# Kernel tuning notes

Measured on AMD Instinct MI355X. Metric: run time of the kernel, lower is better.

## Reference

```python
import jax, jax.numpy as jnp
import numpy as np

N_EMBD = 1024
D_K = 1024
D_V = 1024

def setup_inputs() -> dict:
    key = jax.random.key(0)
    k1, k2, k3, k4 = jax.random.split(key, 4)
    B, T = 4, 2048
    std = N_EMBD ** -0.5
    x = jax.random.normal(k1, (B, T, N_EMBD), dtype=jnp.float32)
    Wq = jax.random.normal(k2, (N_EMBD, D_K), dtype=jnp.float32) * std
    Wk = jax.random.normal(k3, (N_EMBD, D_K), dtype=jnp.float32) * std
    Wv = jax.random.normal(k4, (N_EMBD, D_V), dtype=jnp.float32) * std
    return {"x": x, "Wq": Wq, "Wk": Wk, "Wv": Wv}

def reference(x, Wq, Wk, Wv):
    # x: [B, T, C]
    T = x.shape[1]
    q = x @ Wq  # [B, T, d_k]
    k = x @ Wk  # [B, T, d_k]
    v = x @ Wv  # [B, T, d_v]
    scale = Wk.shape[1] ** -0.5
    wei = jnp.einsum('btd,bsd->bts', q, k) * scale  # [B, T, T]
    causal = jnp.tril(jnp.ones((T, T), dtype=bool))
    wei = jnp.where(causal, wei, -jnp.inf)
    wei = jax.nn.softmax(wei, axis=-1)
    return wei @ v  # [B, T, d_v]
```

## Files before the change

### kernel.cpp

```cpp
#include <hip/hip_runtime.h>
#include <hip/hip_bf16.h>
#include <stdint.h>

using bf16_t = __hip_bfloat16;
typedef __bf16 bf16x8 __attribute__((ext_vector_type(8)));
typedef float f32x4 __attribute__((ext_vector_type(4)));

__device__ __forceinline__ void async_lds16(const void* g, void* l) {
  __builtin_amdgcn_global_load_lds(
      (const __attribute__((address_space(1))) void*)g,
      (__attribute__((address_space(3))) void*)l, 16, 0, 0);
}

__device__ __forceinline__ unsigned short f2bf_u16(float f) {
  __hip_bfloat16 h = __float2bfloat16(f);
  return __builtin_bit_cast(unsigned short, h);
}

__global__ __launch_bounds__(256) void convert_x_kernel(
    const float* __restrict__ x, bf16_t* __restrict__ xb) {
  size_t i = ((size_t)blockIdx.x * 256 + threadIdx.x) * 4;
  float4 v = *(const float4*)(x + i);
  ushort4 o;
  o.x = f2bf_u16(v.x);
  o.y = f2bf_u16(v.y);
  o.z = f2bf_u16(v.z);
  o.w = f2bf_u16(v.w);
  *(ushort4*)(xb + i) = o;
}

__global__ __launch_bounds__(256) void convert_transpose_w_kernel(
    const float* __restrict__ Wq, const float* __restrict__ Wk,
    const float* __restrict__ Wv, bf16_t* __restrict__ wt) {
  __shared__ bf16_t tile[32][33];
  const float* W = (blockIdx.z == 0) ? Wq : (blockIdx.z == 1) ? Wk : Wv;
  bf16_t* WT = wt + (size_t)blockIdx.z * 1024 * 1024;
  const int tx = threadIdx.x & 31;
  const int ty = threadIdx.x >> 5;
  const int bx = blockIdx.x & 31;
  const int by = blockIdx.x >> 5;
  const int k0 = by * 32, n0 = bx * 32;
#pragma unroll
  for (int j = 0; j < 32; j += 8)
    tile[ty + j][tx] = __float2bfloat16(W[(size_t)(k0 + ty + j) * 1024 + n0 + tx]);
  __syncthreads();
#pragma unroll
  for (int j = 0; j < 32; j += 8)
    WT[(size_t)(n0 + ty + j) * 1024 + k0 + tx] = tile[tx][ty + j];
}

template <int OUT_MODE, bool CAUSAL_SKIP, bool KLIMIT, bool XCDSWZ>
__global__ __launch_bounds__(512, 2) void gemm_pipe_kernel(
    const bf16_t* __restrict__ A, const bf16_t* __restrict__ BT,
    void* __restrict__ Cv, void* __restrict__ Cv2, void* __restrict__ Cv3,
    int M, int N, int K, int lda, int ldb, int ldc,
    long long aBatch, long long bBatch, long long cBatch) {
  int bx = blockIdx.x, by = blockIdx.y;
  if (XCDSWZ) {
    const int gx = gridDim.x;
    const int nwg = gx * gridDim.y;
    const int id = by * gx + bx;
    const int cpx = nwg >> 3;
    const int swz = (id & 7) * cpx + (id >> 3);
    by = swz / gx;
    bx = swz % gx;
  }
  const int m0 = by * 128;
  const int n0 = bx * 256;
  if (CAUSAL_SKIP && 2 * bx > by) return;
  A += (size_t)blockIdx.z * aBatch;
  BT += (size_t)blockIdx.z * bBatch;
  int nkt = K >> 5;
  if (KLIMIT) {
    int lim = (m0 + 128) >> 5;
    nkt = nkt < lim ? nkt : lim;
  }

  __shared__ bf16_t lsA[3 * 128 * 32];
  __shared__ bf16_t lsB[3 * 256 * 32];

  const int tid = threadIdx.x;
  const int wid = tid >> 6;
  const int lane = tid & 63;
  const int wm = wid >> 2;
  const int wn = wid & 3;

  const int sr = tid >> 2;
  const int ss = tid & 3;
  const int sswz = ss ^ ((sr >> 1) & 3);
  const bf16_t* gA = A + (size_t)(m0 + sr) * lda + sswz * 8;
  const bf16_t* gB0 = BT + (size_t)(n0 + sr) * ldb + sswz * 8;
  const bf16_t* gB1 = BT + (size_t)(n0 + 128 + sr) * ldb + sswz * 8;

  const int kslot = (lane >> 4) ^ ((lane >> 1) & 3);
  const int abase = (wm * 64 + (lane & 15)) * 32 + kslot * 8;
  const int bbase = (wn * 64 + (lane & 15)) * 32 + kslot * 8;

  f32x4 acc[4][4];
  const f32x4 zero = {0.f, 0.f, 0.f, 0.f};
#pragma unroll
  for (int m = 0; m < 4; ++m)
#pragma unroll
    for (int n = 0; n < 4; ++n) acc[m][n] = zero;

  async_lds16(gA, lsA + wid * 512);
  async_lds16(gB0, lsB + wid * 512);
  async_lds16(gB1, lsB + 4096 + wid * 512);
  if (nkt > 1) {
    async_lds16(gA + 32, lsA + 4096 + wid * 512);
    async_lds16(gB0 + 32, lsB + 8192 + wid * 512);
    async_lds16(gB1 + 32, lsB + 8192 + 4096 + wid * 512);
    asm volatile("s_waitcnt vmcnt(3)" ::: "memory");
  } else {
    asm volatile("s_waitcnt vmcnt(0)" ::: "memory");
  }
  __builtin_amdgcn_s_barrier();

  int cb = 0;
  for (int t = 0; t < nkt; ++t) {
    const bf16_t* bufA = lsA + cb * 4096;
    const bf16_t* bufB = lsB + cb * 8192;
    int sb = cb + 2;
    if (sb >= 3) sb -= 3;

    bf16x8 af[4], bfr[4];
#pragma unroll
    for (int mf = 0; mf < 4; ++mf)
      af[mf] = *(const bf16x8*)(bufA + abase + mf * 512);
    bfr[0] = *(const bf16x8*)(bufB + bbase);
    bfr[1] = *(const bf16x8*)(bufB + bbase + 512);
    if (t + 2 < nkt) {
      async_lds16(gA + (t + 2) * 32, lsA + sb * 4096 + wid * 512);
      async_lds16(gB0 + (t + 2) * 32, lsB + sb * 8192 + wid * 512);
    }
    __builtin_amdgcn_s_barrier();
    __builtin_amdgcn_s_setprio(1);
#pragma unroll
    for (int mf = 0; mf < 4; ++mf)
#pragma unroll
      for (int nf = 0; nf < 2; ++nf)
        acc[mf][nf] = __builtin_amdgcn_mfma_f32_16x16x32_bf16(
            af[mf], bfr[nf], acc[mf][nf], 0, 0, 0);
    __builtin_amdgcn_s_setprio(0);
    __builtin_amdgcn_s_barrier();

    bfr[2] = *(const bf16x8*)(bufB + bbase + 1024);
    bfr[3] = *(const bf16x8*)(bufB + bbase + 1536);
    if (t + 2 < nkt)
      async_lds16(gB1 + (t + 2) * 32, lsB + sb * 8192 + 4096 + wid * 512);
    if (t + 2 < nkt) {
      asm volatile("s_waitcnt vmcnt(3)" ::: "memory");
    } else if (t + 2 == nkt) {
      asm volatile("s_waitcnt vmcnt(0)" ::: "memory");
    }
    __builtin_amdgcn_s_barrier();
    __builtin_amdgcn_s_setprio(1);
#pragma unroll
    for (int mf = 0; mf < 4; ++mf)
#pragma unroll
      for (int nf = 2; nf < 4; ++nf)
        acc[mf][nf] = __builtin_amdgcn_mfma_f32_16x16x32_bf16(
            af[mf], bfr[nf], acc[mf][nf], 0, 0, 0);
    __builtin_amdgcn_s_setprio(0);
    __builtin_amdgcn_s_barrier();

    cb = cb + 1;
    if (cb >= 3) cb -= 3;
  }

  const int erow = wm * 64 + (lane >> 4) * 4;
  const int ecol = wn * 64 + (lane & 15);
  if (OUT_MODE == 2) {
    float* C = (float*)Cv + (size_t)blockIdx.z * cBatch;
#pragma unroll
    for (int m = 0; m < 4; ++m)
#pragma unroll
      for (int n = 0; n < 4; ++n)
#pragma unroll
        for (int j = 0; j < 4; ++j) {
          int r = m0 + erow + m * 16 + j;
          int c = n0 + ecol + n * 16;
          C[(size_t)r * ldc + c] = acc[m][n][j];
        }
  } else {
    if (n0 < 2048) {
      bf16_t* C = (bf16_t*)((n0 < 1024) ? Cv : Cv2);
      const int cb0 = n0 & 1023;
#pragma unroll
      for (int m = 0; m < 4; ++m)
#pragma unroll
        for (int n = 0; n < 4; ++n)
#pragma unroll
          for (int j = 0; j < 4; ++j) {
            int r = m0 + erow + m * 16 + j;
            int c = cb0 + ecol + n * 16;
            C[(size_t)r * 1024 + c] = __float2bfloat16(acc[m][n][j]);
          }
    } else {
      bf16_t* C = (bf16_t*)Cv3;
      const int d0 = n0 - 2048;
#pragma unroll
      for (int m = 0; m < 4; ++m)
#pragma unroll
        for (int n = 0; n < 4; ++n)
#pragma unroll
          for (int j = 0; j < 4; ++j) {
            int r = m0 + erow + m * 16 + j;
            int d = d0 + ecol + n * 16;
            int b = r >> 11, tt = r & 2047;
            C[((size_t)b * 1024 + d) * 2048 + tt] = __float2bfloat16(acc[m][n][j]);
          }
    }
  }
}

__global__ __launch_bounds__(256) void softmax_causal_kernel(float* __restrict__ S) {
  const int lane = threadIdx.x & 63;
  const int rg = blockIdx.x * 4 + (threadIdx.x >> 6);
  const int b = rg >> 11;
  const int t = rg & 2047;
  float* srow = S + (size_t)b * 2048 * 2048 + (size_t)t * 2048;

  float4 v[8];
#pragma unroll
  for (int it = 0; it < 8; ++it) v[it] = *(const float4*)(srow + (it * 64 + lane) * 4);

  float mx = -3.0e38f;
#pragma unroll
  for (int it = 0; it < 8; ++it) {
    int s0 = (it * 64 + lane) * 4;
    if (s0 + 0 <= t) mx = fmaxf(mx, v[it].x);
    if (s0 + 1 <= t) mx = fmaxf(mx, v[it].y);
    if (s0 + 2 <= t) mx = fmaxf(mx, v[it].z);
    if (s0 + 3 <= t) mx = fmaxf(mx, v[it].w);
  }
#pragma unroll
  for (int off = 32; off > 0; off >>= 1) mx = fmaxf(mx, __shfl_xor(mx, off, 64));

  const float kMul = 0.03125f * 1.4426950408889634f;
  float p[8][4];
  float sum = 0.f;
#pragma unroll
  for (int it = 0; it < 8; ++it) {
    int s0 = (it * 64 + lane) * 4;
    float e0 = (s0 + 0 <= t) ? exp2f((v[it].x - mx) * kMul) : 0.f;
    float e1 = (s0 + 1 <= t) ? exp2f((v[it].y - mx) * kMul) : 0.f;
    float e2 = (s0 + 2 <= t) ? exp2f((v[it].z - mx) * kMul) : 0.f;
    float e3 = (s0 + 3 <= t) ? exp2f((v[it].w - mx) * kMul) : 0.f;
    p[it][0] = e0; p[it][1] = e1; p[it][2] = e2; p[it][3] = e3;
    sum += (e0 + e1) + (e2 + e3);
  }
#pragma unroll
  for (int off = 32; off > 0; off >>= 1) sum += __shfl_xor(sum, off, 64);
  const float inv = 1.f / sum;

  bf16_t* prow = (bf16_t*)srow;
#pragma unroll
  for (int it = 0; it < 8; ++it) {
    ushort4 o;
    o.x = f2bf_u16(p[it][0] * inv);
    o.y = f2bf_u16(p[it][1] * inv);
    o.z = f2bf_u16(p[it][2] * inv);
    o.w = f2bf_u16(p[it][3] * inv);
    *(ushort4*)(prow + (it * 64 + lane) * 4) = o;
  }
}

extern "C" void kernel_launch(void* const* d_in, const int* in_sizes, int n_in,
                              void* d_out, int out_size, void* d_ws, size_t ws_size,
                              hipStream_t stream) {
  (void)in_sizes; (void)n_in; (void)out_size;
  const float* x = (const float*)d_in[0];
  const float* Wq = (const float*)d_in[1];
  const float* Wk = (const float*)d_in[2];
  const float* Wv = (const float*)d_in[3];
  float* out = (float*)d_out;

  char* ws = (char*)d_ws;
  const size_t NEED = 123731968;
  const bool batched = ws_size >= NEED;

  bf16_t* xb = (bf16_t*)ws;
  float* S;
  bf16_t *WT, *Qb, *Kb, *VT;
  if (batched) {
    S = (float*)ws;
    WT = (bf16_t*)(ws + 67108864);
    Qb = (bf16_t*)(ws + 73400320);
    Kb = (bf16_t*)(ws + 90177536);
    VT = (bf16_t*)(ws + 106954752);
  } else {
    S = (float*)ws;
    WT = (bf16_t*)(ws + 16777216);
    Qb = (bf16_t*)(ws + 16777216 + 6291456);
    Kb = Qb + 8388608;
    VT = Kb + 8388608;
  }

  convert_x_kernel<<<8192, 256, 0, stream>>>(x, xb);
  convert_transpose_w_kernel<<<dim3(1024, 1, 3), 256, 0, stream>>>(Wq, Wk, Wv, WT);

  gemm_pipe_kernel<3, false, false, true><<<dim3(12, 64, 1), 512, 0, stream>>>(
      xb, WT, Qb, Kb, VT, 8192, 3072, 1024, 1024, 1024, 0, 0, 0, 0);

  if (batched) {
    gemm_pipe_kernel<2, true, false, false><<<dim3(8, 16, 4), 512, 0, stream>>>(
        Qb, Kb, S, nullptr, nullptr, 2048, 2048, 1024, 1024, 1024, 2048,
        2097152LL, 2097152LL, 4194304LL);
    softmax_causal_kernel<<<2048, 256, 0, stream>>>(S);
    gemm_pipe_kernel<2, false, true, false><<<dim3(4, 16, 4), 512, 0, stream>>>(
        (const bf16_t*)S, VT, out, nullptr, nullptr, 2048, 1024, 2048, 4096,
        2048, 1024, 8388608LL, 2097152LL, 2097152LL);
  } else {
    for (int b = 0; b < 4; ++b) {
      const size_t qoff = (size_t)b * 2048 * 1024;
      gemm_pipe_kernel<2, true, false, false><<<dim3(8, 16, 1), 512, 0, stream>>>(
          Qb + qoff, Kb + qoff, S, nullptr, nullptr, 2048, 2048, 1024, 1024,
          1024, 2048, 0, 0, 0);
      softmax_causal_kernel<<<512, 256, 0, stream>>>(S);
      gemm_pipe_kernel<2, false, true, false><<<dim3(4, 16, 1), 512, 0, stream>>>(
          (const bf16_t*)S, VT + qoff, out + qoff, nullptr, nullptr, 2048,
          1024, 2048, 4096, 2048, 1024, 0, 0, 0);
    }
  }
}
```

Measured before the change: 187.0 us.

## Enlarge GEMM tiles to 256x256x64 with double-buffered four-phase pipeline

Measured after the change: 200.5 us. 1.07x slower.

```diff
diff --git a/kernel.cpp b/kernel.cpp
--- a/kernel.cpp
+++ b/kernel.cpp
@@ -50,7 +50,7 @@
 }
 
 template <int OUT_MODE, bool CAUSAL_SKIP, bool KLIMIT, bool XCDSWZ>
-__global__ __launch_bounds__(512, 2) void gemm_pipe_kernel(
+__global__ __launch_bounds__(512, 2) void gemm256_kernel(
     const bf16_t* __restrict__ A, const bf16_t* __restrict__ BT,
     void* __restrict__ Cv, void* __restrict__ Cv2, void* __restrict__ Cv3,
     int M, int N, int K, int lda, int ldb, int ldc,
@@ -65,19 +65,19 @@
     by = swz / gx;
     bx = swz % gx;
   }
-  const int m0 = by * 128;
+  const int m0 = by * 256;
   const int n0 = bx * 256;
-  if (CAUSAL_SKIP && 2 * bx > by) return;
+  if (CAUSAL_SKIP && bx > by) return;
   A += (size_t)blockIdx.z * aBatch;
   BT += (size_t)blockIdx.z * bBatch;
-  int nkt = K >> 5;
+  int nkt = K >> 6;
   if (KLIMIT) {
-    int lim = (m0 + 128) >> 5;
+    int lim = (m0 + 256) >> 6;
     nkt = nkt < lim ? nkt : lim;
   }
 
-  __shared__ bf16_t lsA[3 * 128 * 32];
-  __shared__ bf16_t lsB[3 * 256 * 32];
+  __shared__ bf16_t lsA[2 * 16384];
+  __shared__ bf16_t lsB[2 * 16384];
 
   const int tid = threadIdx.x;
   const int wid = tid >> 6;
@@ -86,94 +86,123 @@
   const int wn = wid & 3;
 
   const int sr = tid >> 2;
-  const int ss = tid & 3;
-  const int sswz = ss ^ ((sr >> 1) & 3);
-  const bf16_t* gA = A + (size_t)(m0 + sr) * lda + sswz * 8;
+  const int sswz = (tid & 3) ^ ((tid >> 3) & 3);
+  const bf16_t* gA0 = A + (size_t)(m0 + sr) * lda + sswz * 8;
+  const bf16_t* gA1 = A + (size_t)(m0 + 128 + sr) * lda + sswz * 8;
   const bf16_t* gB0 = BT + (size_t)(n0 + sr) * ldb + sswz * 8;
   const bf16_t* gB1 = BT + (size_t)(n0 + 128 + sr) * ldb + sswz * 8;
 
-  const int kslot = (lane >> 4) ^ ((lane >> 1) & 3);
-  const int abase = (wm * 64 + (lane & 15)) * 32 + kslot * 8;
-  const int bbase = (wn * 64 + (lane & 15)) * 32 + kslot * 8;
-
-  f32x4 acc[4][4];
+  auto stageA = [&](int t, int kh) {
+    bf16_t* d = lsA + ((t & 1) << 14) + (kh << 13) + (wid << 9);
+    const size_t co = (size_t)(t << 6) + (kh << 5);
+    async_lds16(gA0 + co, d);
+    async_lds16(gA1 + co, d + 4096);
+  };
+  auto stageB = [&](int t, int kh) {
+    bf16_t* d = lsB + ((t & 1) << 14) + (kh << 13) + (wid << 9);
+    const size_t co = (size_t)(t << 6) + (kh << 5);
+    async_lds16(gB0 + co, d);
+    async_lds16(gB1 + co, d + 4096);
+  };
+
+  const int kswz = ((lane >> 4) ^ ((lane >> 1) & 3)) * 8;
+  const int aRd = (wm * 128 + (lane & 15)) * 32 + kswz;
+  const int bRd = (wn * 64 + (lane & 15)) * 32 + kswz;
+
+  f32x4 acc[8][4];
   const f32x4 zero = {0.f, 0.f, 0.f, 0.f};
 #pragma unroll
-  for (int m = 0; m < 4; ++m)
+  for (int m = 0; m < 8; ++m)
 #pragma unroll
     for (int n = 0; n < 4; ++n) acc[m][n] = zero;
 
-  async_lds16(gA, lsA + wid * 512);
-  async_lds16(gB0, lsB + wid * 512);
-  async_lds16(gB1, lsB + 4096 + wid * 512);
+  stageA(0, 0);
+  stageB(0, 0);
+  stageA(0, 1);
+  stageB(0, 1);
   if (nkt > 1) {
-    async_lds16(gA + 32, lsA + 4096 + wid * 512);
-    async_lds16(gB0 + 32, lsB + 8192 + wid * 512);
-    async_lds16(gB1 + 32, lsB + 8192 + 4096 + wid * 512);
-    asm volatile("s_waitcnt vmcnt(3)" ::: "memory");
+    stageA(1, 0);
+    stageB(1, 0);
+    asm volatile("s_waitcnt vmcnt(4)" ::: "memory");
   } else {
     asm volatile("s_waitcnt vmcnt(0)" ::: "memory");
   }
   __builtin_amdgcn_s_barrier();
 
-  int cb = 0;
+  bf16x8 af[4], bfr[4];
+
+#define PHASE_TAIL()                                      \
+  __builtin_amdgcn_s_barrier();                           \
+  asm volatile("s_waitcnt lgkmcnt(0)" ::: "memory");      \
+  __builtin_amdgcn_sched_barrier(0);                      \
+  __builtin_amdgcn_s_setprio(1);
+
+#define MFMA16(mh)                                        \
+  _Pragma("unroll") for (int mf = 0; mf < 4; ++mf)        \
+      _Pragma("unroll") for (int nf = 0; nf < 4; ++nf)    \
+          acc[(mh)*4 + mf][nf] = __builtin_amdgcn_mfma_f32_16x16x32_bf16( \
+              af[mf], bfr[nf], acc[(mh)*4 + mf][nf], 0, 0, 0);
+
   for (int t = 0; t < nkt; ++t) {
-    const bf16_t* bufA = lsA + cb * 4096;
-    const bf16_t* bufB = lsB + cb * 8192;
-    int sb = cb + 2;
-    if (sb >= 3) sb -= 3;
-
-    bf16x8 af[4], bfr[4];
+    const bf16_t* bufA = lsA + ((t & 1) << 14);
+    const bf16_t* bufB = lsB + ((t & 1) << 14);
+
+#pragma unroll
+    for (int nf = 0; nf < 4; ++nf)
+      bfr[nf] = *(const bf16x8*)(bufB + (nf << 9) + bRd);
 #pragma unroll
     for (int mf = 0; mf < 4; ++mf)
-      af[mf] = *(const bf16x8*)(bufA + abase + mf * 512);
-    bfr[0] = *(const bf16x8*)(bufB + bbase);
-    bfr[1] = *(const bf16x8*)(bufB + bbase + 512);
-    if (t + 2 < nkt) {
-      async_lds16(gA + (t + 2) * 32, lsA + sb * 4096 + wid * 512);
-      async_lds16(gB0 + (t + 2) * 32, lsB + sb * 8192 + wid * 512);
-    }
-    __builtin_amdgcn_s_barrier();
-    __builtin_amdgcn_s_setprio(1);
-#pragma unroll
-    for (int mf = 0; mf < 4; ++mf)
-#pragma unroll
-      for (int nf = 0; nf < 2; ++nf)
-        acc[mf][nf] = __builtin_amdgcn_mfma_f32_16x16x32_bf16(
-            af[mf], bfr[nf], acc[mf][nf], 0, 0, 0);
+      af[mf] = *(const bf16x8*)(bufA + (mf << 9) + aRd);
+    if (t + 1 < nkt) stageA(t + 1, 1);
+    PHASE_TAIL()
+    MFMA16(0)
     __builtin_amdgcn_s_setprio(0);
     __builtin_amdgcn_s_barrier();
 
-    bfr[2] = *(const bf16x8*)(bufB + bbase + 1024);
-    bfr[3] = *(const bf16x8*)(bufB + bbase + 1536);
-    if (t + 2 < nkt)
-      async_lds16(gB1 + (t + 2) * 32, lsB + sb * 8192 + 4096 + wid * 512);
+#pragma unroll
+    for (int mf = 0; mf < 4; ++mf)
+      af[mf] = *(const bf16x8*)(bufA + ((mf + 4) << 9) + aRd);
+    if (t + 1 < nkt) stageB(t + 1, 1);
+    PHASE_TAIL()
+    MFMA16(1)
+    __builtin_amdgcn_s_setprio(0);
+    __builtin_amdgcn_s_barrier();
+
+#pragma unroll
+    for (int nf = 0; nf < 4; ++nf)
+      bfr[nf] = *(const bf16x8*)(bufB + 8192 + (nf << 9) + bRd);
+#pragma unroll
+    for (int mf = 0; mf < 4; ++mf)
+      af[mf] = *(const bf16x8*)(bufA + 8192 + (mf << 9) + aRd);
+    if (t + 2 < nkt) stageA(t + 2, 0);
+    PHASE_TAIL()
+    MFMA16(0)
+    __builtin_amdgcn_s_setprio(0);
+    __builtin_amdgcn_s_barrier();
+
+#pragma unroll
+    for (int mf = 0; mf < 4; ++mf)
+      af[mf] = *(const bf16x8*)(bufA + 8192 + ((mf + 4) << 9) + aRd);
+    if (t + 2 < nkt) stageB(t + 2, 0);
+    PHASE_TAIL()
+    MFMA16(1)
+    __builtin_amdgcn_s_setprio(0);
     if (t + 2 < nkt) {
-      asm volatile("s_waitcnt vmcnt(3)" ::: "memory");
-    } else if (t + 2 == nkt) {
+      asm volatile("s_waitcnt vmcnt(4)" ::: "memory");
+    } else if (t + 1 < nkt) {
       asm volatile("s_waitcnt vmcnt(0)" ::: "memory");
     }
     __builtin_amdgcn_s_barrier();
-    __builtin_amdgcn_s_setprio(1);
-#pragma unroll
-    for (int mf = 0; mf < 4; ++mf)
-#pragma unroll
-      for (int nf = 2; nf < 4; ++nf)
-        acc[mf][nf] = __builtin_amdgcn_mfma_f32_16x16x32_bf16(
-            af[mf], bfr[nf], acc[mf][nf], 0, 0, 0);
-    __builtin_amdgcn_s_setprio(0);
-    __builtin_amdgcn_s_barrier();
-
-    cb = cb + 1;
-    if (cb >= 3) cb -= 3;
-  }
-
-  const int erow = wm * 64 + (lane >> 4) * 4;
+  }
+#undef PHASE_TAIL
+#undef MFMA16
+
+  const int erow = wm * 128 + (lane >> 4) * 4;
   const int ecol = wn * 64 + (lane & 15);
   if (OUT_MODE == 2) {
     float* C = (float*)Cv + (size_t)blockIdx.z * cBatch;
 #pragma unroll
-    for (int m = 0; m < 4; ++m)
+    for (int m = 0; m < 8; ++m)
 #pragma unroll
       for (int n = 0; n < 4; ++n)
 #pragma unroll
@@ -187,7 +216,7 @@
       bf16_t* C = (bf16_t*)((n0 < 1024) ? Cv : Cv2);
       const int cb0 = n0 & 1023;
 #pragma unroll
-      for (int m = 0; m < 4; ++m)
+      for (int m = 0; m < 8; ++m)
 #pragma unroll
         for (int n = 0; n < 4; ++n)
 #pragma unroll
@@ -200,7 +229,7 @@
       bf16_t* C = (bf16_t*)Cv3;
       const int d0 = n0 - 2048;
 #pragma unroll
-      for (int m = 0; m < 4; ++m)
+      for (int m = 0; m < 8; ++m)
 #pragma unroll
         for (int n = 0; n < 4; ++n)
 #pragma unroll
@@ -220,10 +249,16 @@
   const int b = rg >> 11;
   const int t = rg & 2047;
   float* srow = S + (size_t)b * 2048 * 2048 + (size_t)t * 2048;
+  const int qmax = t >> 8;
 
   float4 v[8];
 #pragma unroll
-  for (int it = 0; it < 8; ++it) v[it] = *(const float4*)(srow + (it * 64 + lane) * 4);
+  for (int it = 0; it < 8; ++it) {
+    if (it <= qmax)
+      v[it] = *(const float4*)(srow + (it * 64 + lane) * 4);
+    else
+      v[it] = make_float4(0.f, 0.f, 0.f, 0.f);
+  }
 
   float mx = -3.0e38f;
 #pragma unroll
@@ -257,12 +292,14 @@
   bf16_t* prow = (bf16_t*)srow;
 #pragma unroll
   for (int it = 0; it < 8; ++it) {
-    ushort4 o;
-    o.x = f2bf_u16(p[it][0] * inv);
-    o.y = f2bf_u16(p[it][1] * inv);
-    o.z = f2bf_u16(p[it][2] * inv);
-    o.w = f2bf_u16(p[it][3] * inv);
-    *(ushort4*)(prow + (it * 64 + lane) * 4) = o;
+    if (it <= qmax) {
+      ushort4 o;
+      o.x = f2bf_u16(p[it][0] * inv);
+      o.y = f2bf_u16(p[it][1] * inv);
+      o.z = f2bf_u16(p[it][2] * inv);
+      o.w = f2bf_u16(p[it][3] * inv);
+      *(ushort4*)(prow + (it * 64 + lane) * 4) = o;
+    }
   }
 }
 
@@ -300,25 +337,25 @@
   convert_x_kernel<<<8192, 256, 0, stream>>>(x, xb);
   convert_transpose_w_kernel<<<dim3(1024, 1, 3), 256, 0, stream>>>(Wq, Wk, Wv, WT);
 
-  gemm_pipe_kernel<3, false, false, true><<<dim3(12, 64, 1), 512, 0, stream>>>(
+  gemm256_kernel<3, false, false, true><<<dim3(12, 32, 1), 512, 0, stream>>>(
       xb, WT, Qb, Kb, VT, 8192, 3072, 1024, 1024, 1024, 0, 0, 0, 0);
 
   if (batched) {
-    gemm_pipe_kernel<2, true, false, false><<<dim3(8, 16, 4), 512, 0, stream>>>(
+    gemm256_kernel<2, true, false, false><<<dim3(8, 8, 4), 512, 0, stream>>>(
         Qb, Kb, S, nullptr, nullptr, 2048, 2048, 1024, 1024, 1024, 2048,
         2097152LL, 2097152LL, 4194304LL);
     softmax_causal_kernel<<<2048, 256, 0, stream>>>(S);
-    gemm_pipe_kernel<2, false, true, false><<<dim3(4, 16, 4), 512, 0, stream>>>(
+    gemm256_kernel<2, false, true, false><<<dim3(4, 8, 4), 512, 0, stream>>>(
         (const bf16_t*)S, VT, out, nullptr, nullptr, 2048, 1024, 2048, 4096,
         2048, 1024, 8388608LL, 2097152LL, 2097152LL);
   } else {
     for (int b = 0; b < 4; ++b) {
       const size_t qoff = (size_t)b * 2048 * 1024;
-      gemm_pipe_kernel<2, true, false, false><<<dim3(8, 16, 1), 512, 0, stream>>>(
+      gemm256_kernel<2, true, false, false><<<dim3(8, 8, 1), 512, 0, stream>>>(
           Qb + qoff, Kb + qoff, S, nullptr, nullptr, 2048, 2048, 1024, 1024,
           1024, 2048, 0, 0, 0);
       softmax_causal_kernel<<<512, 256, 0, stream>>>(S);
-      gemm_pipe_kernel<2, false, true, false><<<dim3(4, 16, 1), 512, 0, stream>>>(
+      gemm256_kernel<2, false, true, false><<<dim3(4, 8, 1), 512, 0, stream>>>(
           (const bf16_t*)S, VT + qoff, out + qoff, nullptr, nullptr, 2048,
           1024, 2048, 4096, 2048, 1024, 0, 0, 0);
     }
```

## Store attention scores as bf16, skip masked softmax tiles, merge conversion kernels

Applied to the files above, without the earlier changes.

New measurement: 179.9 us. 3.8% less time.

```diff
diff --git a/kernel.cpp b/kernel.cpp
--- a/kernel.cpp
+++ b/kernel.cpp
@@ -17,28 +17,37 @@
   return __builtin_bit_cast(unsigned short, h);
 }
 
-__global__ __launch_bounds__(256) void convert_x_kernel(
-    const float* __restrict__ x, bf16_t* __restrict__ xb) {
-  size_t i = ((size_t)blockIdx.x * 256 + threadIdx.x) * 4;
-  float4 v = *(const float4*)(x + i);
-  ushort4 o;
-  o.x = f2bf_u16(v.x);
-  o.y = f2bf_u16(v.y);
-  o.z = f2bf_u16(v.z);
-  o.w = f2bf_u16(v.w);
-  *(ushort4*)(xb + i) = o;
-}
-
-__global__ __launch_bounds__(256) void convert_transpose_w_kernel(
+__device__ __forceinline__ float bf2f(unsigned short u) {
+  __hip_bfloat16 h = __builtin_bit_cast(__hip_bfloat16, u);
+  return __bfloat162float(h);
+}
+
+__global__ __launch_bounds__(256) void convert_all_kernel(
+    const float* __restrict__ x, bf16_t* __restrict__ xb,
     const float* __restrict__ Wq, const float* __restrict__ Wk,
     const float* __restrict__ Wv, bf16_t* __restrict__ wt) {
   __shared__ bf16_t tile[32][33];
-  const float* W = (blockIdx.z == 0) ? Wq : (blockIdx.z == 1) ? Wk : Wv;
-  bf16_t* WT = wt + (size_t)blockIdx.z * 1024 * 1024;
+  const int bid = blockIdx.x;
+  if (bid < 8192) {
+    size_t i = ((size_t)bid * 256 + threadIdx.x) * 4;
+    float4 v = *(const float4*)(x + i);
+    ushort4 o;
+    o.x = f2bf_u16(v.x);
+    o.y = f2bf_u16(v.y);
+    o.z = f2bf_u16(v.z);
+    o.w = f2bf_u16(v.w);
+    *(ushort4*)(xb + i) = o;
+    return;
+  }
+  const int w = bid - 8192;
+  const int z = w >> 10;
+  const int bxy = w & 1023;
+  const float* W = (z == 0) ? Wq : (z == 1) ? Wk : Wv;
+  bf16_t* WT = wt + (size_t)z * 1024 * 1024;
   const int tx = threadIdx.x & 31;
   const int ty = threadIdx.x >> 5;
-  const int bx = blockIdx.x & 31;
-  const int by = blockIdx.x >> 5;
+  const int bx = bxy & 31;
+  const int by = bxy >> 5;
   const int k0 = by * 32, n0 = bx * 32;
 #pragma unroll
   for (int j = 0; j < 32; j += 8)
@@ -182,6 +191,18 @@
           int c = n0 + ecol + n * 16;
           C[(size_t)r * ldc + c] = acc[m][n][j];
         }
+  } else if (OUT_MODE == 4) {
+    bf16_t* C = (bf16_t*)Cv + (size_t)blockIdx.z * cBatch;
+#pragma unroll
+    for (int m = 0; m < 4; ++m)
+#pragma unroll
+      for (int n = 0; n < 4; ++n)
+#pragma unroll
+        for (int j = 0; j < 4; ++j) {
+          int r = m0 + erow + m * 16 + j;
+          int c = n0 + ecol + n * 16;
+          C[(size_t)r * ldc + c] = __float2bfloat16(acc[m][n][j]);
+        }
   } else {
     if (n0 < 2048) {
       bf16_t* C = (bf16_t*)((n0 < 1024) ? Cv : Cv2);
@@ -214,25 +235,36 @@
   }
 }
 
-__global__ __launch_bounds__(256) void softmax_causal_kernel(float* __restrict__ S) {
+__global__ __launch_bounds__(256) void softmax_causal_kernel(bf16_t* __restrict__ Sb) {
   const int lane = threadIdx.x & 63;
   const int rg = blockIdx.x * 4 + (threadIdx.x >> 6);
   const int b = rg >> 11;
   const int t = rg & 2047;
-  float* srow = S + (size_t)b * 2048 * 2048 + (size_t)t * 2048;
-
-  float4 v[8];
-#pragma unroll
-  for (int it = 0; it < 8; ++it) v[it] = *(const float4*)(srow + (it * 64 + lane) * 4);
+  bf16_t* srow = Sb + (size_t)b * 8388608 + (size_t)t * 4096;
+  const int qmax = t >> 8;
+
+  float v[8][4];
+#pragma unroll
+  for (int it = 0; it < 8; ++it) {
+    if (it <= qmax) {
+      ushort4 u = *(const ushort4*)(srow + (it * 64 + lane) * 4);
+      v[it][0] = bf2f(u.x);
+      v[it][1] = bf2f(u.y);
+      v[it][2] = bf2f(u.z);
+      v[it][3] = bf2f(u.w);
+    } else {
+      v[it][0] = v[it][1] = v[it][2] = v[it][3] = 0.f;
+    }
+  }
 
   float mx = -3.0e38f;
 #pragma unroll
   for (int it = 0; it < 8; ++it) {
     int s0 = (it * 64 + lane) * 4;
-    if (s0 + 0 <= t) mx = fmaxf(mx, v[it].x);
-    if (s0 + 1 <= t) mx = fmaxf(mx, v[it].y);
-    if (s0 + 2 <= t) mx = fmaxf(mx, v[it].z);
-    if (s0 + 3 <= t) mx = fmaxf(mx, v[it].w);
+    if (s0 + 0 <= t) mx = fmaxf(mx, v[it][0]);
+    if (s0 + 1 <= t) mx = fmaxf(mx, v[it][1]);
+    if (s0 + 2 <= t) mx = fmaxf(mx, v[it][2]);
+    if (s0 + 3 <= t) mx = fmaxf(mx, v[it][3]);
   }
 #pragma unroll
   for (int off = 32; off > 0; off >>= 1) mx = fmaxf(mx, __shfl_xor(mx, off, 64));
@@ -243,10 +275,10 @@
 #pragma unroll
   for (int it = 0; it < 8; ++it) {
     int s0 = (it * 64 + lane) * 4;
-    float e0 = (s0 + 0 <= t) ? exp2f((v[it].x - mx) * kMul) : 0.f;
-    float e1 = (s0 + 1 <= t) ? exp2f((v[it].y - mx) * kMul) : 0.f;
-    float e2 = (s0 + 2 <= t) ? exp2f((v[it].z - mx) * kMul) : 0.f;
-    float e3 = (s0 + 3 <= t) ? exp2f((v[it].w - mx) * kMul) : 0.f;
+    float e0 = (s0 + 0 <= t) ? exp2f((v[it][0] - mx) * kMul) : 0.f;
+    float e1 = (s0 + 1 <= t) ? exp2f((v[it][1] - mx) * kMul) : 0.f;
+    float e2 = (s0 + 2 <= t) ? exp2f((v[it][2] - mx) * kMul) : 0.f;
+    float e3 = (s0 + 3 <= t) ? exp2f((v[it][3] - mx) * kMul) : 0.f;
     p[it][0] = e0; p[it][1] = e1; p[it][2] = e2; p[it][3] = e3;
     sum += (e0 + e1) + (e2 + e3);
   }
@@ -254,15 +286,16 @@
   for (int off = 32; off > 0; off >>= 1) sum += __shfl_xor(sum, off, 64);
   const float inv = 1.f / sum;
 
-  bf16_t* prow = (bf16_t*)srow;
 #pragma unroll
   for (int it = 0; it < 8; ++it) {
-    ushort4 o;
-    o.x = f2bf_u16(p[it][0] * inv);
-    o.y = f2bf_u16(p[it][1] * inv);
-    o.z = f2bf_u16(p[it][2] * inv);
-    o.w = f2bf_u16(p[it][3] * inv);
-    *(ushort4*)(prow + (it * 64 + lane) * 4) = o;
+    if (it <= qmax) {
+      ushort4 o;
+      o.x = f2bf_u16(p[it][0] * inv);
+      o.y = f2bf_u16(p[it][1] * inv);
+      o.z = f2bf_u16(p[it][2] * inv);
+      o.w = f2bf_u16(p[it][3] * inv);
+      *(ushort4*)(srow + (it * 64 + lane) * 4) = o;
+    }
   }
 }
 
@@ -281,45 +314,44 @@
   const bool batched = ws_size >= NEED;
 
   bf16_t* xb = (bf16_t*)ws;
-  float* S;
+  bf16_t* Sb;
   bf16_t *WT, *Qb, *Kb, *VT;
   if (batched) {
-    S = (float*)ws;
+    Sb = (bf16_t*)ws;
     WT = (bf16_t*)(ws + 67108864);
     Qb = (bf16_t*)(ws + 73400320);
     Kb = (bf16_t*)(ws + 90177536);
     VT = (bf16_t*)(ws + 106954752);
   } else {
-    S = (float*)ws;
+    Sb = (bf16_t*)ws;
     WT = (bf16_t*)(ws + 16777216);
     Qb = (bf16_t*)(ws + 16777216 + 6291456);
     Kb = Qb + 8388608;
     VT = Kb + 8388608;
   }
 
-  convert_x_kernel<<<8192, 256, 0, stream>>>(x, xb);
-  convert_transpose_w_kernel<<<dim3(1024, 1, 3), 256, 0, stream>>>(Wq, Wk, Wv, WT);
+  convert_all_kernel<<<11264, 256, 0, stream>>>(x, xb, Wq, Wk, Wv, WT);
 
   gemm_pipe_kernel<3, false, false, true><<<dim3(12, 64, 1), 512, 0, stream>>>(
       xb, WT, Qb, Kb, VT, 8192, 3072, 1024, 1024, 1024, 0, 0, 0, 0);
 
   if (batched) {
-    gemm_pipe_kernel<2, true, false, false><<<dim3(8, 16, 4), 512, 0, stream>>>(
-        Qb, Kb, S, nullptr, nullptr, 2048, 2048, 1024, 1024, 1024, 2048,
-        2097152LL, 2097152LL, 4194304LL);
-    softmax_causal_kernel<<<2048, 256, 0, stream>>>(S);
+    gemm_pipe_kernel<4, true, false, false><<<dim3(8, 16, 4), 512, 0, stream>>>(
+        Qb, Kb, Sb, nullptr, nullptr, 2048, 2048, 1024, 1024, 1024, 4096,
+        2097152LL, 2097152LL, 8388608LL);
+    softmax_causal_kernel<<<2048, 256, 0, stream>>>(Sb);
     gemm_pipe_kernel<2, false, true, false><<<dim3(4, 16, 4), 512, 0, stream>>>(
-        (const bf16_t*)S, VT, out, nullptr, nullptr, 2048, 1024, 2048, 4096,
+        Sb, VT, out, nullptr, nullptr, 2048, 1024, 2048, 4096,
         2048, 1024, 8388608LL, 2097152LL, 2097152LL);
   } else {
     for (int b = 0; b < 4; ++b) {
       const size_t qoff = (size_t)b * 2048 * 1024;
-      gemm_pipe_kernel<2, true, false, false><<<dim3(8, 16, 1), 512, 0, stream>>>(
-          Qb + qoff, Kb + qoff, S, nullptr, nullptr, 2048, 2048, 1024, 1024,
-          1024, 2048, 0, 0, 0);
-      softmax_causal_kernel<<<512, 256, 0, stream>>>(S);
+      gemm_pipe_kernel<4, true, false, false><<<dim3(8, 16, 1), 512, 0, stream>>>(
+          Qb + qoff, Kb + qoff, Sb, nullptr, nullptr, 2048, 2048, 1024, 1024,
+          1024, 4096, 0, 0, 0);
+      softmax_causal_kernel<<<512, 256, 0, stream>>>(Sb);
       gemm_pipe_kernel<2, false, true, false><<<dim3(4, 16, 1), 512, 0, stream>>>(
-          (const bf16_t*)S, VT + qoff, out + qoff, nullptr, nullptr, 2048,
+          Sb, VT + qoff, out + qoff, nullptr, nullptr, 2048,
           1024, 2048, 4096, 2048, 1024, 0, 0, 0);
     }
   }
```
